# Optimization experiments

Hardware: AMD Instinct MI355X
Metric: run time of the kernel (lower is better)

Reference implementation:

```python
import jax, jax.numpy as jnp
import numpy as np

N, E, F_NODE, F_EDGE, HID, B, GDIM, ACT = 50000, 1600000, 32, 8, 256, 64, 16, 64
N_HIDDEN_LAYERS = 3


def setup_inputs() -> dict:
    key = jax.random.key(0)
    ks = jax.random.split(key, 16)
    x = jax.random.normal(ks[0], (N, F_NODE), jnp.float32)
    edge_index = jax.random.randint(ks[1], (2, E), 0, N, jnp.int64)
    edge_attr = jax.random.normal(ks[2], (E, F_EDGE), jnp.float32)
    batch = jnp.sort(jax.random.randint(ks[3], (N,), 0, B, jnp.int64))
    global_feats = jax.random.normal(ks[4], (B, GDIM), jnp.float32)
    s = lambda *d: 1.0 / np.sqrt(d[-2])
    # layer 0: node_feat -> hidden ; layers 1..3: hidden -> hidden
    We0 = jax.random.normal(ks[5], (F_EDGE, F_NODE), jnp.float32) * (1.0 / np.sqrt(F_EDGE))
    W0 = jax.random.normal(ks[6], (F_NODE, HID), jnp.float32) * (1.0 / np.sqrt(F_NODE))
    b0 = jnp.zeros((HID,), jnp.float32)
    We = jax.random.normal(ks[7], (N_HIDDEN_LAYERS, F_EDGE, HID), jnp.float32) * (1.0 / np.sqrt(F_EDGE))
    W = jax.random.normal(ks[8], (N_HIDDEN_LAYERS, HID, HID), jnp.float32) * (1.0 / np.sqrt(HID))
    b = jnp.zeros((N_HIDDEN_LAYERS, HID), jnp.float32)
    Wp = jax.random.normal(ks[9], (HID + GDIM, ACT), jnp.float32) * (1.0 / np.sqrt(HID + GDIM))
    bp = jnp.zeros((ACT,), jnp.float32)
    Wv = jax.random.normal(ks[10], (HID + GDIM, 1), jnp.float32) * (1.0 / np.sqrt(HID + GDIM))
    bv = jnp.zeros((1,), jnp.float32)
    return {"x": x, "edge_attr": edge_attr, "global_feats": global_feats,
            "We0": We0, "W0": W0, "b0": b0, "We": We, "W": W, "b": b,
            "Wp": Wp, "bp": bp, "Wv": Wv, "bv": bv,
            "edge_index": edge_index, "batch": batch}


def reference(x, edge_attr, global_feats, We0, W0, b0, We, W, b, Wp, bp, Wv, bv, edge_index, batch):
    src, dst = edge_index[0], edge_index[1]
    n_nodes = x.shape[0]
    n_graphs = global_feats.shape[0]

    def conv(h, We_l, W_l, b_l):
        # GINE-style: message relu(x_j + proj(e_ij)), sum-aggregate, node update MLP
        m = jax.nn.relu(h[src] + edge_attr @ We_l)            # [E, d]
        agg = jax.ops.segment_sum(m, dst, num_segments=n_nodes)
        return jax.nn.relu((h + agg) @ W_l + b_l)             # [N, hidden]

    h = conv(x, We0, W0, b0)
    for i in range(We.shape[0]):
        h = conv(h, We[i], W[i], b[i])

    counts = jax.ops.segment_sum(jnp.ones((n_nodes, 1), h.dtype), batch, num_segments=n_graphs)
    pooled = jax.ops.segment_sum(h, batch, num_segments=n_graphs) / jnp.maximum(counts, 1.0)
    feats = jnp.concatenate([pooled, global_feats], axis=-1)  # [B, hidden+gdim]
    logits = feats @ Wp + bp                                  # [B, max_action_dim]
    value = feats @ Wv + bv                                   # [B, 1]
    return logits, value
```

## Files before the change

### kernel.cpp

```cpp
#include <hip/hip_runtime.h>
#include <hip/hip_bf16.h>

#define NNODES 50000
#define NEDGES 1600000
#define FNODE 32
#define FEDGE 8
#define HIDD 256
#define NGRAPH 64
#define GDIM 16
#define NACT 64
#define FEATD (HIDD + GDIM)
#define PCH 8

typedef short bf16x8 __attribute__((ext_vector_type(8)));
typedef float f32x4 __attribute__((ext_vector_type(4)));
typedef __bf16 bf16x2 __attribute__((ext_vector_type(2)));


__device__ inline float bfl(uint u) {
  union { uint i; float f; } v; v.i = u << 16; return v.f;
}
__device__ inline float bfh(uint u) {
  union { uint i; float f; } v; v.i = u & 0xffff0000u; return v.f;
}
__device__ inline float bf1(ushort u) {
  union { uint i; float f; } v; v.i = ((uint)u) << 16; return v.f;
}
__device__ inline ushort f2b(float a) {
  __hip_bfloat16 h = __float2bfloat16(a);
  return *(ushort*)&h;
}
__device__ inline uint packbf(float a, float b) {
  return (uint)f2b(a) | ((uint)f2b(b) << 16);
}

__device__ inline float dot2bf(uint a, uint b, float c) {
#if defined(__has_builtin)
#if __has_builtin(__builtin_amdgcn_fdot2_f32_bf16)
  union { uint u; bf16x2 v; } ua, ub;
  ua.u = a; ub.u = b;
  return __builtin_amdgcn_fdot2_f32_bf16(ua.v, ub.v, c, false);
#else
  return fmaf(bfl(a), bfl(b), fmaf(bfh(a), bfh(b), c));
#endif
#else
  return fmaf(bfl(a), bfl(b), fmaf(bfh(a), bfh(b), c));
#endif
}


__global__ void k_zero_i32(int* __restrict__ p, int n) {
  int i = blockIdx.x * blockDim.x + threadIdx.x;
  if (i < n) p[i] = 0;
}

__global__ void k_hist(const int* __restrict__ dst, int* __restrict__ off) {
  int e = blockIdx.x * blockDim.x + threadIdx.x;
  if (e < NEDGES) atomicAdd(&off[dst[e] + 1], 1);
}

__global__ void k_scan1(int* __restrict__ data, int n, int* __restrict__ sums) {
  __shared__ int buf[1024];
  int gid = blockIdx.x * 1024 + threadIdx.x;
  int v = (gid < n) ? data[gid] : 0;
  buf[threadIdx.x] = v;
  __syncthreads();
  for (int d = 1; d < 1024; d <<= 1) {
    int t = (threadIdx.x >= d) ? buf[threadIdx.x - d] : 0;
    __syncthreads();
    buf[threadIdx.x] += t;
    __syncthreads();
  }
  if (gid < n) data[gid] = buf[threadIdx.x];
  if (threadIdx.x == 1023) sums[blockIdx.x] = buf[1023];
}

__global__ void k_scan2(int* __restrict__ sums, int nb) {
  int run = 0;
  for (int i = 0; i < nb; ++i) { run += sums[i]; sums[i] = run; }
}

__global__ void k_scan3(int* __restrict__ data, int n, const int* __restrict__ sums,
                        int* __restrict__ cur) {
  int gid = blockIdx.x * 1024 + threadIdx.x;
  if (gid < n) {
    int v = data[gid];
    if (blockIdx.x > 0) v += sums[blockIdx.x - 1];
    data[gid] = v;
    if (gid < NNODES) cur[gid] = v;
  }
}

__global__ void k_scatter(const int* __restrict__ src, const int* __restrict__ dst,
                          int* __restrict__ cur, const float* __restrict__ ea,
                          int* __restrict__ csr_src, ushort* __restrict__ eab) {
  int e = blockIdx.x * blockDim.x + threadIdx.x;
  if (e >= NEDGES) return;
  int d = dst[e];
  int pos = atomicAdd(&cur[d], 1);
  csr_src[pos] = src[e];
  float4 a = *(const float4*)&ea[(size_t)e * FEDGE];
  float4 b = *(const float4*)&ea[(size_t)e * FEDGE + 4];
  uint4 o;
  o.x = packbf(a.x, a.y);
  o.y = packbf(a.z, a.w);
  o.z = packbf(b.x, b.y);
  o.w = packbf(b.z, b.w);
  *(uint4*)&eab[(size_t)pos * FEDGE] = o;
}


__global__ void k_cvt_x(const float* __restrict__ x, ushort* __restrict__ xb) {
  int i = blockIdx.x * blockDim.x + threadIdx.x;
  if (i >= NNODES * FNODE / 4) return;
  float4 v = *(const float4*)&x[(size_t)i * 4];
  uint2 o;
  o.x = packbf(v.x, v.y);
  o.y = packbf(v.z, v.w);
  *(uint2*)&xb[(size_t)i * 4] = o;
}


__global__ void k_pack_wep(const float* __restrict__ We0, const float* __restrict__ We,
                           uint* __restrict__ wep0, uint* __restrict__ wep) {
  int t = blockIdx.x * blockDim.x + threadIdx.x;
  if (t < 128) {
    int k2 = t >> 5, c = t & 31;
    wep0[t] = packbf(We0[(2 * k2) * FNODE + c], We0[(2 * k2 + 1) * FNODE + c]);
  } else if (t < 128 + 3 * 1024) {
    int u = t - 128;
    int l = u >> 10;
    int r = u & 1023;
    int k2 = r >> 8, c = r & 255;
    const float* Wl = We + (size_t)l * FEDGE * HIDD;
    wep[u] = packbf(Wl[(2 * k2) * HIDD + c], Wl[(2 * k2 + 1) * HIDD + c]);
  }
}

__global__ void k_pack_w(const float* __restrict__ W0, const float* __restrict__ W,
                         ushort* __restrict__ wp0, ushort* __restrict__ wp) {
  int t = blockIdx.x * blockDim.x + threadIdx.x;
  if (t < 1024) {
    int lane = t & 63;
    int nf = t >> 6;
    int col = nf * 16 + (lane & 15);
    int k0 = (lane >> 4) * 8;
    ushort o[8];
#pragma unroll
    for (int i = 0; i < 8; ++i) o[i] = f2b(W0[(size_t)(k0 + i) * HIDD + col]);
    *(uint4*)&wp0[(size_t)t * 8] = *(uint4*)o;
  } else if (t < 1024 + 3 * 8192) {
    int u = t - 1024;
    int l = u / 8192;
    int r = u - l * 8192;
    int lane = r & 63;
    int frag = r >> 6;
    int nf = frag & 15, ks = frag >> 4;
    int col = nf * 16 + (lane & 15);
    int k0 = ks * 32 + (lane >> 4) * 8;
    const float* Wl = W + (size_t)l * HIDD * HIDD;
    ushort o[8];
#pragma unroll
    for (int i = 0; i < 8; ++i) o[i] = f2b(Wl[(size_t)(k0 + i) * HIDD + col]);
    *(uint4*)&wp[(size_t)u * 8] = *(uint4*)o;
  }
}


__global__ __launch_bounds__(256) void k_edge32(
    const float* __restrict__ x, const ushort* __restrict__ xb,
    const uint4* __restrict__ eab4, const uint* __restrict__ wep0,
    const int* __restrict__ off, const int* __restrict__ csr_src,
    ushort* __restrict__ t0b) {
  int wid = __builtin_amdgcn_readfirstlane(
      (int)((blockIdx.x * blockDim.x + threadIdx.x) >> 6));
  if (wid >= NNODES) return;
  int lane = threadIdx.x & 63;
  int j = lane >> 5;
  int c = lane & 31;
  uint w0 = wep0[c], w1 = wep0[32 + c], w2 = wep0[64 + c], w3 = wep0[96 + c];
  int s0 = off[wid], s1 = off[wid + 1];
  float acc = 0.f;
  int e = s0 + j;
  for (; e + 6 < s1; e += 8) {
    int sA = csr_src[e], sB = csr_src[e + 2], sC = csr_src[e + 4], sD = csr_src[e + 6];
    ushort hA = xb[(size_t)sA * FNODE + c];
    ushort hB = xb[(size_t)sB * FNODE + c];
    ushort hC = xb[(size_t)sC * FNODE + c];
    ushort hD = xb[(size_t)sD * FNODE + c];
    uint4 eA = eab4[e];
    uint4 eB = eab4[e + 2];
    uint4 eC = eab4[e + 4];
    uint4 eD = eab4[e + 6];
    float pr;
#define B32(hu, eu)                 \
    pr = bf1(hu);                   \
    pr = dot2bf(eu.x, w0, pr);      \
    pr = dot2bf(eu.y, w1, pr);      \
    pr = dot2bf(eu.z, w2, pr);      \
    pr = dot2bf(eu.w, w3, pr);      \
    acc += fmaxf(pr, 0.f);
    B32(hA, eA) B32(hB, eB) B32(hC, eC) B32(hD, eD)
  }
  for (; e < s1; e += 2) {
    int s = csr_src[e];
    ushort hu = xb[(size_t)s * FNODE + c];
    uint4 eu = eab4[e];
    float pr;
    B32(hu, eu)
#undef B32
  }
  acc += __shfl_xor(acc, 32);
  if (j == 0) t0b[wid * FNODE + c] = f2b(x[wid * FNODE + c] + acc);
}


__device__ inline void body_dot(uint2 hu, uint4 eu, const uint4 wq[4], float4& acc) {
  float4 pr;
  pr.x = bfl(hu.x);
  pr.y = bfh(hu.x);
  pr.z = bfl(hu.y);
  pr.w = bfh(hu.y);
  pr.x = dot2bf(eu.x, wq[0].x, pr.x);
  pr.x = dot2bf(eu.y, wq[1].x, pr.x);
  pr.x = dot2bf(eu.z, wq[2].x, pr.x);
  pr.x = dot2bf(eu.w, wq[3].x, pr.x);
  pr.y = dot2bf(eu.x, wq[0].y, pr.y);
  pr.y = dot2bf(eu.y, wq[1].y, pr.y);
  pr.y = dot2bf(eu.z, wq[2].y, pr.y);
  pr.y = dot2bf(eu.w, wq[3].y, pr.y);
  pr.z = dot2bf(eu.x, wq[0].z, pr.z);
  pr.z = dot2bf(eu.y, wq[1].z, pr.z);
  pr.z = dot2bf(eu.z, wq[2].z, pr.z);
  pr.z = dot2bf(eu.w, wq[3].z, pr.z);
  pr.w = dot2bf(eu.x, wq[0].w, pr.w);
  pr.w = dot2bf(eu.y, wq[1].w, pr.w);
  pr.w = dot2bf(eu.z, wq[2].w, pr.w);
  pr.w = dot2bf(eu.w, wq[3].w, pr.w);
  acc.x += fmaxf(pr.x, 0.f);
  acc.y += fmaxf(pr.y, 0.f);
  acc.z += fmaxf(pr.z, 0.f);
  acc.w += fmaxf(pr.w, 0.f);
}

#define EDGE_BLOCK(U)                                                       \
  for (; e + (U) <= s1; e += (U)) {                                         \
    int s[U];                                                               \
    uint2 h[U];                                                             \
    uint4 E[U];                                                             \
    _Pragma("unroll") for (int u = 0; u < (U); ++u) s[u] = csr_src[e + u];  \
    _Pragma("unroll") for (int u = 0; u < (U); ++u)                         \
        h[u] = *(const uint2*)&hb[(size_t)s[u] * HIDD + c];                 \
    _Pragma("unroll") for (int u = 0; u < (U); ++u) E[u] = eab4[e + u];     \
    _Pragma("unroll") for (int u = 0; u < (U); ++u)                         \
        body_dot(h[u], E[u], wq, (u & 1) ? acc1 : acc0);                    \
  }

__global__ __launch_bounds__(256) void k_edge256(
    const ushort* __restrict__ hb, const uint4* __restrict__ eab4,
    const uint* __restrict__ wepl, const int* __restrict__ off,
    const int* __restrict__ csr_src, ushort* __restrict__ tb) {
  int wid = __builtin_amdgcn_readfirstlane(
      (int)((blockIdx.x * blockDim.x + threadIdx.x) >> 6));
  if (wid >= NNODES) return;
  int lane = threadIdx.x & 63;
  int c = lane * 4;
  uint4 wq[4];
#pragma unroll
  for (int k2 = 0; k2 < 4; ++k2) wq[k2] = *(const uint4*)&wepl[k2 * HIDD + c];
  int s0 = off[wid], s1 = off[wid + 1];
  float4 acc0 = {0.f, 0.f, 0.f, 0.f}, acc1 = {0.f, 0.f, 0.f, 0.f};
  int e = s0;
  EDGE_BLOCK(16)
  EDGE_BLOCK(8)
  EDGE_BLOCK(4)
  for (; e < s1; ++e) {
    int s = csr_src[e];
    uint2 hu = *(const uint2*)&hb[(size_t)s * HIDD + c];
    uint4 eu = eab4[e];
    body_dot(hu, eu, wq, acc0);
  }

  uint2 su = *(const uint2*)&hb[(size_t)wid * HIDD + c];
  float4 o;
  o.x = bfl(su.x) + acc0.x + acc1.x;
  o.y = bfh(su.x) + acc0.y + acc1.y;
  o.z = bfl(su.y) + acc0.z + acc1.z;
  o.w = bfh(su.y) + acc0.w + acc1.w;
  uint2 ob;
  ob.x = packbf(o.x, o.y);
  ob.y = packbf(o.z, o.w);
  *(uint2*)&tb[(size_t)wid * HIDD + c] = ob;
}
#undef EDGE_BLOCK


template <int K>
__global__ __launch_bounds__(512) void k_gemm_mfma(
    const ushort* __restrict__ Tb, const ushort* __restrict__ Wp,
    const float* __restrict__ bias, ushort* __restrict__ outb, int nrows) {
  constexpr int CPR = K / 8;
  constexpr int SWZ = (CPR - 1) & 7;
  __shared__ ushort tl[128 * K];
  const int tid = threadIdx.x;
  const int r0 = blockIdx.x * 128;
  for (int ch = tid; ch < 128 * CPR; ch += 512) {
    int row = ch / CPR;
    int cb = ch - row * CPR;
    uint4 v = make_uint4(0, 0, 0, 0);
    if (r0 + row < nrows) v = *(const uint4*)&Tb[(size_t)(r0 + row) * K + cb * 8];
    *(uint4*)&tl[(size_t)(row * CPR + (cb ^ (row & SWZ))) * 8] = v;
  }
  __syncthreads();
  const int wave = tid >> 6;
  const int lane = tid & 63;
  const int arow = wave * 16 + (lane & 15);
  const int kgrp = lane >> 4;
  f32x4 acc[16];
#pragma unroll
  for (int nf = 0; nf < 16; ++nf) acc[nf] = (f32x4){0.f, 0.f, 0.f, 0.f};
#pragma unroll
  for (int ks = 0; ks < K / 32; ++ks) {
    int cb = ks * 4 + kgrp;
    bf16x8 af = *(const bf16x8*)&tl[(size_t)(arow * CPR + (cb ^ (arow & SWZ))) * 8];
#pragma unroll
    for (int nf = 0; nf < 16; ++nf) {
      bf16x8 bfg = *(const bf16x8*)&Wp[(((size_t)ks * 16 + nf) * 64 + lane) * 8];
      acc[nf] = __builtin_amdgcn_mfma_f32_16x16x32_bf16(af, bfg, acc[nf], 0, 0, 0);
    }
  }
  const int ocol0 = lane & 15;
  const int orow0 = r0 + wave * 16 + (lane >> 4) * 4;
#pragma unroll
  for (int nf = 0; nf < 16; ++nf) {
    int col = nf * 16 + ocol0;
    float bv = bias[col];
#pragma unroll
    for (int r = 0; r < 4; ++r) {
      int row = orow0 + r;
      if (row < nrows) outb[(size_t)row * HIDD + col] = f2b(fmaxf(acc[nf][r] + bv, 0.f));
    }
  }
}


__global__ void k_pool_partial(const ushort* __restrict__ hb, const int* __restrict__ batch,
                               float* __restrict__ fp) {
  int b = blockIdx.x >> 3;
  int j = blockIdx.x & 7;
  __shared__ int srange[2];
  if (threadIdx.x < 2) {
    int target = b + threadIdx.x;
    int lo = 0, hi = NNODES;
    while (lo < hi) {
      int mid = (lo + hi) >> 1;
      if (batch[mid] < target) lo = mid + 1; else hi = mid;
    }
    srange[threadIdx.x] = lo;
  }
  __syncthreads();
  int s = srange[0], eend = srange[1];
  int len = eend - s;
  int cs = s + (int)((long long)len * j / PCH);
  int ce = s + (int)((long long)len * (j + 1) / PCH);
  int col = threadIdx.x;
  float acc = 0.f;
  for (int n = cs; n < ce; ++n) acc += bf1(hb[(size_t)n * HIDD + col]);
  fp[((size_t)j * NGRAPH + b) * HIDD + col] = acc;
}

__global__ void k_pool_final(const float* __restrict__ fp, const int* __restrict__ batch,
                             const float* __restrict__ gf, float* __restrict__ feats) {
  int b = blockIdx.x;
  __shared__ int srange[2];
  if (threadIdx.x < 2) {
    int target = b + threadIdx.x;
    int lo = 0, hi = NNODES;
    while (lo < hi) {
      int mid = (lo + hi) >> 1;
      if (batch[mid] < target) lo = mid + 1; else hi = mid;
    }
    srange[threadIdx.x] = lo;
  }
  __syncthreads();
  int col = threadIdx.x;
  float acc = 0.f;
#pragma unroll
  for (int j = 0; j < PCH; ++j) acc += fp[((size_t)j * NGRAPH + b) * HIDD + col];
  float cnt = fmaxf((float)(srange[1] - srange[0]), 1.0f);
  feats[b * FEATD + col] = acc / cnt;
  if (col < GDIM) feats[b * FEATD + HIDD + col] = gf[b * GDIM + col];
}


__global__ void k_heads(const float* __restrict__ feats, const float* __restrict__ Wp,
                        const float* __restrict__ bp, const float* __restrict__ Wv,
                        const float* __restrict__ bv, float* __restrict__ out) {
  int b = blockIdx.x;
  int t = threadIdx.x;
  __shared__ float f[FEATD];
  for (int i = t; i < FEATD; i += 64) f[i] = feats[b * FEATD + i];
  __syncthreads();
  float acc = bp[t];
  for (int k = 0; k < FEATD; ++k) acc = fmaf(f[k], Wp[k * NACT + t], acc);
  out[b * NACT + t] = acc;
  float pv = 0.f;
  for (int k = t; k < FEATD; k += 64) pv = fmaf(f[k], Wv[k], pv);
#pragma unroll
  for (int d = 32; d > 0; d >>= 1) pv += __shfl_down(pv, d);
  if (t == 0) out[NGRAPH * NACT + b] = pv + bv[0];
}


extern "C" void kernel_launch(void* const* d_in, const int* in_sizes, int n_in,
                              void* d_out, int out_size, void* d_ws, size_t ws_size,
                              hipStream_t stream) {
  const float* x   = (const float*)d_in[0];
  const float* ea  = (const float*)d_in[1];
  const float* gf  = (const float*)d_in[2];
  const float* We0 = (const float*)d_in[3];
  const float* W0  = (const float*)d_in[4];
  const float* b0  = (const float*)d_in[5];
  const float* We  = (const float*)d_in[6];
  const float* W   = (const float*)d_in[7];
  const float* bb  = (const float*)d_in[8];
  const float* Wp  = (const float*)d_in[9];
  const float* bp  = (const float*)d_in[10];
  const float* Wv  = (const float*)d_in[11];
  const float* bv  = (const float*)d_in[12];
  const int* eidx  = (const int*)d_in[13];
  const int* batch = (const int*)d_in[14];
  const int* esrc = eidx;
  const int* edst = eidx + NEDGES;

  char* w = (char*)d_ws;
  size_t p = 0;
  auto take = [&](size_t bytes) {
    size_t r = p;
    p += (bytes + 255) & ~(size_t)255;
    return r;
  };
  int* off      = (int*)(w + take((NNODES + 1) * 4));
  int* cur      = (int*)(w + take(NNODES * 4));
  int* sums     = (int*)(w + take(1024));
  int* csr_src  = (int*)(w + take((size_t)NEDGES * 4));
  ushort* eab   = (ushort*)(w + take((size_t)NEDGES * FEDGE * 2));
  ushort* t0b   = (ushort*)(w + take((size_t)NNODES * FNODE * 2));
  ushort* xb    = (ushort*)(w + take((size_t)NNODES * FNODE * 2));
  ushort* tb    = (ushort*)(w + take((size_t)NNODES * HIDD * 2));
  ushort* hb    = (ushort*)(w + take((size_t)NNODES * HIDD * 2));
  uint* wep0    = (uint*)(w + take(128 * 4));
  uint* wepb    = (uint*)(w + take(3 * 1024 * 4));
  ushort* wp0   = (ushort*)(w + take((size_t)1024 * 8 * 2));
  ushort* wpb   = (ushort*)(w + take((size_t)3 * 8192 * 8 * 2));
  float* fp     = (float*)(w + take((size_t)PCH * NGRAPH * HIDD * 4));
  float* feats  = (float*)(w + take((size_t)NGRAPH * FEATD * 4));
  if (p > ws_size) return;

  k_zero_i32<<<(NNODES + 1 + 255) / 256, 256, 0, stream>>>(off, NNODES + 1);
  k_hist<<<(NEDGES + 255) / 256, 256, 0, stream>>>(edst, off);
  int n_scan = NNODES + 1;
  int nb_scan = (n_scan + 1023) / 1024;
  k_scan1<<<nb_scan, 1024, 0, stream>>>(off, n_scan, sums);
  k_scan2<<<1, 1, 0, stream>>>(sums, nb_scan);
  k_scan3<<<nb_scan, 1024, 0, stream>>>(off, n_scan, sums, cur);
  k_scatter<<<(NEDGES + 255) / 256, 256, 0, stream>>>(esrc, edst, cur, ea, csr_src, eab);

  k_pack_wep<<<(128 + 3 * 1024 + 255) / 256, 256, 0, stream>>>(We0, We, wep0, wepb);
  k_pack_w<<<(1024 + 3 * 8192 + 255) / 256, 256, 0, stream>>>(W0, W, wp0, wpb);
  k_cvt_x<<<(NNODES * FNODE / 4 + 255) / 256, 256, 0, stream>>>(x, xb);

  const int gemm_grid = (NNODES + 127) / 128;

  k_edge32<<<NNODES / 4, 256, 0, stream>>>(x, xb, (const uint4*)eab, wep0, off,
                                           csr_src, t0b);
  k_gemm_mfma<FNODE><<<gemm_grid, 512, 0, stream>>>(t0b, wp0, b0, hb, NNODES);

  for (int l = 0; l < 3; ++l) {
    k_edge256<<<NNODES / 4, 256, 0, stream>>>(hb, (const uint4*)eab, wepb + l * 1024,
                                              off, csr_src, tb);
    k_gemm_mfma<HIDD><<<gemm_grid, 512, 0, stream>>>(
        tb, wpb + (size_t)l * 8192 * 8, bb + (size_t)l * HIDD, hb, NNODES);
  }

  k_pool_partial<<<NGRAPH * PCH, HIDD, 0, stream>>>(hb, batch, fp);
  k_pool_final<<<NGRAPH, HIDD, 0, stream>>>(fp, batch, gf, feats);
  k_heads<<<NGRAPH, 64, 0, stream>>>(feats, Wp, bp, Wv, bv, (float*)d_out);
}
```

Measured before the change: 749.4 us.

## Fuse prep kernels, drop scan2 launch, and load GEMM A-fragments directly from global

```diff
diff --git a/kernel.cpp b/kernel.cpp
--- a/kernel.cpp
+++ b/kernel.cpp
@@ -75,17 +75,13 @@
   if (threadIdx.x == 1023) sums[blockIdx.x] = buf[1023];
 }
 
-__global__ void k_scan2(int* __restrict__ sums, int nb) {
-  int run = 0;
-  for (int i = 0; i < nb; ++i) { run += sums[i]; sums[i] = run; }
-}
-
 __global__ void k_scan3(int* __restrict__ data, int n, const int* __restrict__ sums,
                         int* __restrict__ cur) {
+  int base = 0;
+  for (int i = 0; i < (int)blockIdx.x; ++i) base += sums[i];
   int gid = blockIdx.x * 1024 + threadIdx.x;
   if (gid < n) {
-    int v = data[gid];
-    if (blockIdx.x > 0) v += sums[blockIdx.x - 1];
+    int v = data[gid] + base;
     data[gid] = v;
     if (gid < NNODES) cur[gid] = v;
   }
@@ -110,59 +106,65 @@
 }
 
 
-__global__ void k_cvt_x(const float* __restrict__ x, ushort* __restrict__ xb) {
+#define CVT_N (NNODES * FNODE / 4)
+#define WEP_N (128 + 3 * 1024)
+#define WP_N (1024 + 3 * 8192)
+
+__global__ void k_prep(const float* __restrict__ x, ushort* __restrict__ xb,
+                       const float* __restrict__ We0, const float* __restrict__ We,
+                       uint* __restrict__ wep0, uint* __restrict__ wep,
+                       const float* __restrict__ W0, const float* __restrict__ W,
+                       ushort* __restrict__ wp0, ushort* __restrict__ wp) {
   int i = blockIdx.x * blockDim.x + threadIdx.x;
-  if (i >= NNODES * FNODE / 4) return;
-  float4 v = *(const float4*)&x[(size_t)i * 4];
-  uint2 o;
-  o.x = packbf(v.x, v.y);
-  o.y = packbf(v.z, v.w);
-  *(uint2*)&xb[(size_t)i * 4] = o;
-}
-
-
-__global__ void k_pack_wep(const float* __restrict__ We0, const float* __restrict__ We,
-                           uint* __restrict__ wep0, uint* __restrict__ wep) {
-  int t = blockIdx.x * blockDim.x + threadIdx.x;
-  if (t < 128) {
-    int k2 = t >> 5, c = t & 31;
-    wep0[t] = packbf(We0[(2 * k2) * FNODE + c], We0[(2 * k2 + 1) * FNODE + c]);
-  } else if (t < 128 + 3 * 1024) {
-    int u = t - 128;
-    int l = u >> 10;
-    int r = u & 1023;
-    int k2 = r >> 8, c = r & 255;
-    const float* Wl = We + (size_t)l * FEDGE * HIDD;
-    wep[u] = packbf(Wl[(2 * k2) * HIDD + c], Wl[(2 * k2 + 1) * HIDD + c]);
-  }
-}
-
-__global__ void k_pack_w(const float* __restrict__ W0, const float* __restrict__ W,
-                         ushort* __restrict__ wp0, ushort* __restrict__ wp) {
-  int t = blockIdx.x * blockDim.x + threadIdx.x;
-  if (t < 1024) {
-    int lane = t & 63;
-    int nf = t >> 6;
-    int col = nf * 16 + (lane & 15);
-    int k0 = (lane >> 4) * 8;
-    ushort o[8];
-#pragma unroll
-    for (int i = 0; i < 8; ++i) o[i] = f2b(W0[(size_t)(k0 + i) * HIDD + col]);
-    *(uint4*)&wp0[(size_t)t * 8] = *(uint4*)o;
-  } else if (t < 1024 + 3 * 8192) {
-    int u = t - 1024;
-    int l = u / 8192;
-    int r = u - l * 8192;
-    int lane = r & 63;
-    int frag = r >> 6;
-    int nf = frag & 15, ks = frag >> 4;
-    int col = nf * 16 + (lane & 15);
-    int k0 = ks * 32 + (lane >> 4) * 8;
-    const float* Wl = W + (size_t)l * HIDD * HIDD;
-    ushort o[8];
-#pragma unroll
-    for (int i = 0; i < 8; ++i) o[i] = f2b(Wl[(size_t)(k0 + i) * HIDD + col]);
-    *(uint4*)&wp[(size_t)u * 8] = *(uint4*)o;
+  if (i < CVT_N) {
+    float4 v = *(const float4*)&x[(size_t)i * 4];
+    uint2 o;
+    o.x = packbf(v.x, v.y);
+    o.y = packbf(v.z, v.w);
+    *(uint2*)&xb[(size_t)i * 4] = o;
+    return;
+  }
+  i -= CVT_N;
+  if (i < WEP_N) {
+    if (i < 128) {
+      int k2 = i >> 5, c = i & 31;
+      wep0[i] = packbf(We0[(2 * k2) * FNODE + c], We0[(2 * k2 + 1) * FNODE + c]);
+    } else {
+      int u = i - 128;
+      int l = u >> 10;
+      int r = u & 1023;
+      int k2 = r >> 8, c = r & 255;
+      const float* Wl = We + (size_t)l * FEDGE * HIDD;
+      wep[u] = packbf(Wl[(2 * k2) * HIDD + c], Wl[(2 * k2 + 1) * HIDD + c]);
+    }
+    return;
+  }
+  i -= WEP_N;
+  if (i < WP_N) {
+    if (i < 1024) {
+      int lane = i & 63;
+      int nf = i >> 6;
+      int col = nf * 16 + (lane & 15);
+      int k0 = (lane >> 4) * 8;
+      ushort o[8];
+#pragma unroll
+      for (int q = 0; q < 8; ++q) o[q] = f2b(W0[(size_t)(k0 + q) * HIDD + col]);
+      *(uint4*)&wp0[(size_t)i * 8] = *(uint4*)o;
+    } else {
+      int u = i - 1024;
+      int l = u / 8192;
+      int r = u - l * 8192;
+      int lane = r & 63;
+      int frag = r >> 6;
+      int nf = frag & 15, ks = frag >> 4;
+      int col = nf * 16 + (lane & 15);
+      int k0 = ks * 32 + (lane >> 4) * 8;
+      const float* Wl = W + (size_t)l * HIDD * HIDD;
+      ushort o[8];
+#pragma unroll
+      for (int q = 0; q < 8; ++q) o[q] = f2b(Wl[(size_t)(k0 + q) * HIDD + col]);
+      *(uint4*)&wp[(size_t)u * 8] = *(uint4*)o;
+    }
   }
 }
 
@@ -296,33 +298,21 @@
 
 
 template <int K>
-__global__ __launch_bounds__(512) void k_gemm_mfma(
+__global__ __launch_bounds__(256) void k_gemm_mfma(
     const ushort* __restrict__ Tb, const ushort* __restrict__ Wp,
     const float* __restrict__ bias, ushort* __restrict__ outb, int nrows) {
-  constexpr int CPR = K / 8;
-  constexpr int SWZ = (CPR - 1) & 7;
-  __shared__ ushort tl[128 * K];
-  const int tid = threadIdx.x;
-  const int r0 = blockIdx.x * 128;
-  for (int ch = tid; ch < 128 * CPR; ch += 512) {
-    int row = ch / CPR;
-    int cb = ch - row * CPR;
-    uint4 v = make_uint4(0, 0, 0, 0);
-    if (r0 + row < nrows) v = *(const uint4*)&Tb[(size_t)(r0 + row) * K + cb * 8];
-    *(uint4*)&tl[(size_t)(row * CPR + (cb ^ (row & SWZ))) * 8] = v;
-  }
-  __syncthreads();
-  const int wave = tid >> 6;
-  const int lane = tid & 63;
-  const int arow = wave * 16 + (lane & 15);
+  const int gwave = (int)((blockIdx.x * blockDim.x + threadIdx.x) >> 6);
+  const int row0 = gwave * 16;
+  if (row0 >= nrows) return;
+  const int lane = threadIdx.x & 63;
+  const int arow = row0 + (lane & 15);
   const int kgrp = lane >> 4;
   f32x4 acc[16];
 #pragma unroll
   for (int nf = 0; nf < 16; ++nf) acc[nf] = (f32x4){0.f, 0.f, 0.f, 0.f};
 #pragma unroll
   for (int ks = 0; ks < K / 32; ++ks) {
-    int cb = ks * 4 + kgrp;
-    bf16x8 af = *(const bf16x8*)&tl[(size_t)(arow * CPR + (cb ^ (arow & SWZ))) * 8];
+    bf16x8 af = *(const bf16x8*)&Tb[(size_t)arow * K + ks * 32 + kgrp * 8];
 #pragma unroll
     for (int nf = 0; nf < 16; ++nf) {
       bf16x8 bfg = *(const bf16x8*)&Wp[(((size_t)ks * 16 + nf) * 64 + lane) * 8];
@@ -330,7 +320,7 @@
     }
   }
   const int ocol0 = lane & 15;
-  const int orow0 = r0 + wave * 16 + (lane >> 4) * 4;
+  const int orow0 = row0 + (lane >> 4) * 4;
 #pragma unroll
   for (int nf = 0; nf < 16; ++nf) {
     int col = nf * 16 + ocol0;
@@ -462,24 +452,22 @@
   int n_scan = NNODES + 1;
   int nb_scan = (n_scan + 1023) / 1024;
   k_scan1<<<nb_scan, 1024, 0, stream>>>(off, n_scan, sums);
-  k_scan2<<<1, 1, 0, stream>>>(sums, nb_scan);
   k_scan3<<<nb_scan, 1024, 0, stream>>>(off, n_scan, sums, cur);
   k_scatter<<<(NEDGES + 255) / 256, 256, 0, stream>>>(esrc, edst, cur, ea, csr_src, eab);
 
-  k_pack_wep<<<(128 + 3 * 1024 + 255) / 256, 256, 0, stream>>>(We0, We, wep0, wepb);
-  k_pack_w<<<(1024 + 3 * 8192 + 255) / 256, 256, 0, stream>>>(W0, W, wp0, wpb);
-  k_cvt_x<<<(NNODES * FNODE / 4 + 255) / 256, 256, 0, stream>>>(x, xb);
-
-  const int gemm_grid = (NNODES + 127) / 128;
+  k_prep<<<(CVT_N + WEP_N + WP_N + 255) / 256, 256, 0, stream>>>(
+      x, xb, We0, We, wep0, wepb, W0, W, wp0, wpb);
+
+  const int gemm_grid = (NNODES / 16 + 3) / 4;
 
   k_edge32<<<NNODES / 4, 256, 0, stream>>>(x, xb, (const uint4*)eab, wep0, off,
                                            csr_src, t0b);
-  k_gemm_mfma<FNODE><<<gemm_grid, 512, 0, stream>>>(t0b, wp0, b0, hb, NNODES);
+  k_gemm_mfma<FNODE><<<gemm_grid, 256, 0, stream>>>(t0b, wp0, b0, hb, NNODES);
 
   for (int l = 0; l < 3; ++l) {
     k_edge256<<<NNODES / 4, 256, 0, stream>>>(hb, (const uint4*)eab, wepb + l * 1024,
                                               off, csr_src, tb);
-    k_gemm_mfma<HIDD><<<gemm_grid, 512, 0, stream>>>(
+    k_gemm_mfma<HIDD><<<gemm_grid, 256, 0, stream>>>(
         tb, wpb + (size_t)l * 8192 * 8, bb + (size_t)l * HIDD, hb, NNODES);
   }
 
```

Result: slower. 797.5 us (+6.4%).
